# Performance work log

Measured on AMD Instinct MI355X. Metric: run time of the kernel, lower is better.

## Reference

```python
import jax, jax.numpy as jnp
import numpy as np

N = 4096      # nodes
DIM = 256     # in/out channels
H = 8         # heads
C = DIM       # per-head channels (PyG TransformerConv: out_channels per head)
EPS = 1e-5    # LayerNorm eps
P_EDGE = 0.01 # adjacency density -> avg in-degree ~41


def setup_inputs() -> dict:
    key = jax.random.key(0)
    ks = jax.random.split(key, 12)
    x = jax.random.normal(ks[0], (1, N, DIM), jnp.float32)
    # sparse random graph encoded densely (dense_to_sparse extracts nonzeros)
    adj_mat = (jax.random.uniform(ks[1], (1, N, N)) < P_EDGE).astype(jnp.float32)
    s = 1.0 / np.sqrt(DIM)
    Wq = jax.random.normal(ks[2], (DIM, H * C), jnp.float32) * s
    Wk = jax.random.normal(ks[3], (DIM, H * C), jnp.float32) * s
    Wv = jax.random.normal(ks[4], (DIM, H * C), jnp.float32) * s
    bq = jax.random.normal(ks[5], (H * C,), jnp.float32) * 0.01
    bk = jax.random.normal(ks[6], (H * C,), jnp.float32) * 0.01
    bv = jax.random.normal(ks[7], (H * C,), jnp.float32) * 0.01
    Wskip = jax.random.normal(ks[8], (DIM, DIM), jnp.float32) * s
    bskip = jax.random.normal(ks[9], (DIM,), jnp.float32) * 0.01
    gamma = jnp.ones((DIM,), jnp.float32)
    beta = jnp.zeros((DIM,), jnp.float32)
    return dict(x=x, adj_mat=adj_mat, Wq=Wq, bq=bq, Wk=Wk, bk=bk, Wv=Wv, bv=bv,
                Wskip=Wskip, bskip=bskip, gamma=gamma, beta=beta)


def reference(x, adj_mat, Wq, bq, Wk, bk, Wv, bv, Wskip, bskip, gamma, beta):
    xs = x[0]            # [N, DIM]
    adj = adj_mat[0]     # [N, N]; adj[j, i] != 0 => edge j -> i (source_to_target)
    q = (xs @ Wq + bq).reshape(N, H, C)
    k = (xs @ Wk + bk).reshape(N, H, C)
    v = (xs @ Wv + bv).reshape(N, H, C)
    # scaled dot-product attention restricted to graph edges
    scores = jnp.einsum('ihc,jhc->hij', q, k) / jnp.sqrt(jnp.float32(C))  # [H,N,N]
    mask = (adj.T != 0.0)[None]  # [1, i_target, j_source]
    neg = jnp.finfo(scores.dtype).min
    attn = jax.nn.softmax(jnp.where(mask, scores, neg), axis=-1)
    # nodes with no in-edges aggregate zero messages (scatter semantics)
    has_nbr = mask.any(axis=-1, keepdims=True)  # [1, N, 1]
    attn = jnp.where(has_nbr, attn, 0.0)
    agg = jnp.einsum('hij,jhc->ihc', attn, v)  # [N, H, C]
    out = agg.mean(axis=1)                      # concat=False -> head mean, [N, DIM]
    out = out + xs @ Wskip + bskip              # root_weight skip connection
    mu = out.mean(axis=-1, keepdims=True)
    var = ((out - mu) ** 2).mean(axis=-1, keepdims=True)
    out = (out - mu) * jax.lax.rsqrt(var + EPS) * gamma + beta  # LayerNorm
    out = out + xs                               # residual
    return out[None]  # [1, N, DIM]
```

## Files before the change

### kernel.cpp

```cpp
#include <hip/hip_runtime.h>
#include <hip/hip_bf16.h>

#define NN   4096
#define DIMM 256
#define HH   8
#define HC   2048
#define CAP  128

typedef short  bf16x8 __attribute__((ext_vector_type(8)));
typedef float  f32x4  __attribute__((ext_vector_type(4)));
typedef float  f32x2  __attribute__((ext_vector_type(2)));

__device__ __forceinline__ float bfbits(unsigned int u) {
  union { unsigned int u; float f; } un; un.u = u; return un.f;
}
__device__ __forceinline__ unsigned short f2bf(float f) {
  union { float f; unsigned int u; } un; un.f = f;
  unsigned int r = un.u + 0x7fffu + ((un.u >> 16) & 1u);
  return (unsigned short)(r >> 16);
}
__device__ __forceinline__ void gload16(const void* g, void* l) {
  __builtin_amdgcn_global_load_lds(
      (const __attribute__((address_space(1))) unsigned int*)g,
      (__attribute__((address_space(3))) unsigned int*)l, 16, 0, 0);
}

__global__ __launch_bounds__(256) void build_edges_kernel(
    const float4* __restrict__ adj4, int* __restrict__ deg, int* __restrict__ nbr) {
  const int stride = gridDim.x * blockDim.x;
  for (int e4 = blockIdx.x * blockDim.x + threadIdx.x; e4 < NN * NN / 4; e4 += stride) {
    const float4 a = adj4[e4];
    if (a.x != 0.f || a.y != 0.f || a.z != 0.f || a.w != 0.f) {
      const int e = e4 << 2;
      const int j = e >> 12;
      const int ib = e & (NN - 1);
      if (a.x != 0.f) { int s = atomicAdd(&deg[ib + 0], 1); if (s < CAP) nbr[(ib + 0) * CAP + s] = j; }
      if (a.y != 0.f) { int s = atomicAdd(&deg[ib + 1], 1); if (s < CAP) nbr[(ib + 1) * CAP + s] = j; }
      if (a.z != 0.f) { int s = atomicAdd(&deg[ib + 2], 1); if (s < CAP) nbr[(ib + 2) * CAP + s] = j; }
      if (a.w != 0.f) { int s = atomicAdd(&deg[ib + 3], 1); if (s < CAP) nbr[(ib + 3) * CAP + s] = j; }
    }
  }
}

__global__ __launch_bounds__(128) void sort_nbr_kernel(
    const int* __restrict__ deg, int* __restrict__ nbr) {
  const int i = blockIdx.x, t = threadIdx.x;
  __shared__ int sl[CAP];
  int d = deg[i];
  if (d > CAP) d = CAP;
  if (d <= 1) return;
  sl[t] = (t < d) ? nbr[i * CAP + t] : 0x7fffffff;
  __syncthreads();
  for (int ksz = 2; ksz <= CAP; ksz <<= 1) {
    for (int jsz = ksz >> 1; jsz > 0; jsz >>= 1) {
      const int ixj = t ^ jsz;
      if (ixj > t) {
        const int a = sl[t], b = sl[ixj];
        const bool up = ((t & ksz) == 0);
        if ((up && a > b) || (!up && a < b)) { sl[t] = b; sl[ixj] = a; }
      }
      __syncthreads();
    }
  }
  if (t < d) nbr[i * CAP + t] = sl[t];
}

__global__ __launch_bounds__(256) void cast_x_kernel(
    const float* __restrict__ x, unsigned short* __restrict__ xb) {
  const int gid = blockIdx.x * 256 + threadIdx.x;
  const int m = gid >> 5, c = gid & 31;
  const float4 a = *(const float4*)&x[(size_t)m * 256 + c * 8];
  const float4 b = *(const float4*)&x[(size_t)m * 256 + c * 8 + 4];
  union { unsigned short u[8]; uint4 v; } o;
  o.u[0] = f2bf(a.x); o.u[1] = f2bf(a.y); o.u[2] = f2bf(a.z); o.u[3] = f2bf(a.w);
  o.u[4] = f2bf(b.x); o.u[5] = f2bf(b.y); o.u[6] = f2bf(b.z); o.u[7] = f2bf(b.w);
  const int cs = (c & 24) | ((c & 7) ^ (m & 7));
  *(uint4*)&xb[(size_t)m * 256 + cs * 8] = o.v;
}

__global__ __launch_bounds__(256) void tcast_w_kernel(
    const float* __restrict__ W0, const float* __restrict__ W1,
    const float* __restrict__ W2, unsigned short* __restrict__ T0,
    unsigned short* __restrict__ T1, unsigned short* __restrict__ T2, int Nw) {
  const float* W = blockIdx.z == 0 ? W0 : blockIdx.z == 1 ? W1 : W2;
  unsigned short* T = blockIdx.z == 0 ? T0 : blockIdx.z == 1 ? T1 : T2;
  __shared__ float Tf[64][68];
  const int t = threadIdx.x;
  const int n0 = blockIdx.x * 64, k0 = blockIdx.y * 64;
  const int kk0 = t >> 4, nc = t & 15;
#pragma unroll
  for (int r = 0; r < 4; ++r) {
    const int kk = kk0 + r * 16;
    const float4 a = *(const float4*)&W[(size_t)(k0 + kk) * Nw + n0 + nc * 4];
    Tf[kk][nc * 4 + 0] = a.x; Tf[kk][nc * 4 + 1] = a.y;
    Tf[kk][nc * 4 + 2] = a.z; Tf[kk][nc * 4 + 3] = a.w;
  }
  __syncthreads();
  const int n = t >> 2, cp = t & 3;
#pragma unroll
  for (int qq = 0; qq < 2; ++qq) {
    const int cc = cp * 2 + qq;
    union { unsigned short u[8]; uint4 v; } o;
#pragma unroll
    for (int e = 0; e < 8; ++e) o.u[e] = f2bf(Tf[cc * 8 + e][n]);
    const int ng = n0 + n;
    const int co = cc ^ (ng & 7);
    *(uint4*)&T[(size_t)ng * 256 + blockIdx.y * 64 + co * 8] = o.v;
  }
}

template <int BF16OUT>
__global__ __launch_bounds__(256) void mfma_gemm_kernel(
    const unsigned short* __restrict__ Abf,
    const unsigned short* __restrict__ B0, const unsigned short* __restrict__ B1,
    const unsigned short* __restrict__ B2,
    const float* __restrict__ bias0, const float* __restrict__ bias1,
    const float* __restrict__ bias2,
    void* __restrict__ C0v, void* __restrict__ C1v, void* __restrict__ C2v,
    int Nc) {
  const unsigned short* Bm = blockIdx.z == 0 ? B0 : blockIdx.z == 1 ? B1 : B2;
  const float* bias = blockIdx.z == 0 ? bias0 : blockIdx.z == 1 ? bias1 : bias2;
  void* Cv = blockIdx.z == 0 ? C0v : blockIdx.z == 1 ? C1v : C2v;

  __shared__ unsigned short lds[2 * 128 * 64];
  unsigned short* As = lds;
  unsigned short* Bs = lds + 128 * 64;

  const int t = threadIdx.x, l = t & 63, w = t >> 6;
  const int m0 = blockIdx.y * 128, n0 = blockIdx.x * 128;
  const int wm = w >> 1, wn = w & 1;

  const f32x4 zero = {0.f, 0.f, 0.f, 0.f};
  f32x4 acc[4][4];
#pragma unroll
  for (int fm = 0; fm < 4; ++fm)
#pragma unroll
    for (int fn = 0; fn < 4; ++fn) acc[fm][fn] = zero;

  for (int kb = 0; kb < 4; ++kb) {
#pragma unroll
    for (int r = 0; r < 4; ++r) {
      const int rr = r * 8 + (l >> 3), ch = l & 7;
      gload16(Abf + (size_t)(m0 + w * 32 + rr) * 256 + kb * 64 + ch * 8,
              As + w * 2048 + r * 512);
      gload16(Bm + (size_t)(n0 + w * 32 + rr) * 256 + kb * 64 + ch * 8,
              Bs + w * 2048 + r * 512);
    }
    __syncthreads();

#pragma unroll
    for (int s = 0; s < 2; ++s) {
      const int chab = (4 * s + (l >> 4)) ^ (l & 7);
      bf16x8 af[4], bfr[4];
#pragma unroll
      for (int fm = 0; fm < 4; ++fm) {
        const int row = wm * 64 + fm * 16 + (l & 15);
        af[fm] = *(const bf16x8*)&As[row * 64 + chab * 8];
      }
#pragma unroll
      for (int fn = 0; fn < 4; ++fn) {
        const int row = wn * 64 + fn * 16 + (l & 15);
        bfr[fn] = *(const bf16x8*)&Bs[row * 64 + chab * 8];
      }
#pragma unroll
      for (int fm = 0; fm < 4; ++fm)
#pragma unroll
        for (int fn = 0; fn < 4; ++fn)
          acc[fm][fn] = __builtin_amdgcn_mfma_f32_16x16x32_bf16(
              af[fm], bfr[fn], acc[fm][fn], 0, 0, 0);
    }
    __syncthreads();
  }

  float bv[4];
#pragma unroll
  for (int fn = 0; fn < 4; ++fn) bv[fn] = bias[n0 + wn * 64 + fn * 16 + (l & 15)];

  if (BF16OUT) {
    unsigned short* Cc = (unsigned short*)Cv;
#pragma unroll
    for (int fm = 0; fm < 4; ++fm) {
      const int colc = wn * 64 + (l & 15);
#pragma unroll
      for (int fn = 0; fn < 4; ++fn) {
        const int col = colc + fn * 16;
#pragma unroll
        for (int r = 0; r < 4; ++r) {
          const int row = wm * 64 + fm * 16 + (l >> 4) * 4 + r;
          const int pos = ((col >> 3) ^ (row & 15)) * 8 + (col & 7);
          lds[row * 128 + pos] = f2bf(acc[fm][fn][r] + bv[fn]);
        }
      }
    }
    __syncthreads();
#pragma unroll
    for (int r2 = 0; r2 < 8; ++r2) {
      const int idx = r2 * 256 + t;
      const int row = idx >> 4, ch = idx & 15;
      *(uint4*)&Cc[(size_t)(m0 + row) * Nc + n0 + ch * 8] =
          *(const uint4*)&lds[row * 128 + (ch ^ (row & 15)) * 8];
    }
  } else {
    float* Cc = (float*)Cv;
#pragma unroll
    for (int fm = 0; fm < 4; ++fm)
#pragma unroll
      for (int fn = 0; fn < 4; ++fn)
#pragma unroll
        for (int r = 0; r < 4; ++r) {
          const int row = wm * 64 + fm * 16 + (l >> 4) * 4 + r;
          const int col = wn * 64 + fn * 16 + (l & 15);
          Cc[(size_t)(m0 + row) * Nc + n0 + col] = acc[fm][fn][r] + bv[fn];
        }
  }
}

__global__ __launch_bounds__(256) void cast8_kernel(
    const unsigned short* __restrict__ in, unsigned char* __restrict__ out8, int n8) {
  const int idx = blockIdx.x * 256 + threadIdx.x;
  if (idx >= n8) return;
  const uint4 w = *(const uint4*)&in[(size_t)idx * 8];
  const float f0 = bfbits(w.x << 16), f1 = bfbits(w.x & 0xffff0000u);
  const float f2 = bfbits(w.y << 16), f3 = bfbits(w.y & 0xffff0000u);
  const float f4 = bfbits(w.z << 16), f5 = bfbits(w.z & 0xffff0000u);
  const float f6 = bfbits(w.w << 16), f7 = bfbits(w.w & 0xffff0000u);
  unsigned int lo = __builtin_amdgcn_cvt_pk_fp8_f32(f0, f1, 0, false);
  lo = __builtin_amdgcn_cvt_pk_fp8_f32(f2, f3, lo, true);
  unsigned int hi = __builtin_amdgcn_cvt_pk_fp8_f32(f4, f5, 0, false);
  hi = __builtin_amdgcn_cvt_pk_fp8_f32(f6, f7, hi, true);
  uint2 o; o.x = lo; o.y = hi;
  *(uint2*)&out8[(size_t)idx * 8] = o;
}

__global__ __launch_bounds__(256) void attn_ln_kernel(
    const unsigned short* __restrict__ q, const unsigned char* __restrict__ k8,
    const unsigned char* __restrict__ v8, const float* __restrict__ skip,
    const float* __restrict__ x, const int* __restrict__ deg,
    const int* __restrict__ nbr, const float* __restrict__ gamma,
    const float* __restrict__ beta, float* __restrict__ out) {
  const int i = blockIdx.x;
  const int t = threadIdx.x;
  const int lane = t & 63, wave = t >> 6;
  const int h = lane >> 3, sub = lane & 7;

  __shared__ int slist[CAP];
  __shared__ float sc[CAP * HH];
  __shared__ float wacc[4][2][DIMM];
  __shared__ float mred[HH], lred[HH];
  __shared__ float w1[4], w2[4];

  int d = deg[i];
  if (d > CAP) d = CAP;

  if (t < CAP) slist[t] = (t < d) ? nbr[i * CAP + t] : 0;

  float qf[32];
  {
    const uint4* qp = (const uint4*)&q[(size_t)i * HC + (h << 8) + (sub << 5)];
#pragma unroll
    for (int b = 0; b < 4; ++b) {
      const uint4 w = qp[b];
      qf[b * 8 + 0] = bfbits(w.x << 16); qf[b * 8 + 1] = bfbits(w.x & 0xffff0000u);
      qf[b * 8 + 2] = bfbits(w.y << 16); qf[b * 8 + 3] = bfbits(w.y & 0xffff0000u);
      qf[b * 8 + 4] = bfbits(w.z << 16); qf[b * 8 + 5] = bfbits(w.z & 0xffff0000u);
      qf[b * 8 + 6] = bfbits(w.w << 16); qf[b * 8 + 7] = bfbits(w.w & 0xffff0000u);
    }
  }
  __syncthreads();

  {
    const size_t hoff = (size_t)(h << 8) + (sub << 5);
    int n = wave;
    uint4 c0, c1;
    if (n < d) {
      const uint4* kp = (const uint4*)&k8[(size_t)slist[n] * HC + hoff];
      c0 = kp[0]; c1 = kp[1];
    }
    while (n < d) {
      const int nn = n + 4;
      uint4 p0, p1;
      if (nn < d) {
        const uint4* kp = (const uint4*)&k8[(size_t)slist[nn] * HC + hoff];
        p0 = kp[0]; p1 = kp[1];
      }
      float s = 0.f;
      const unsigned int cw[8] = {c0.x, c0.y, c0.z, c0.w, c1.x, c1.y, c1.z, c1.w};
#pragma unroll
      for (int b = 0; b < 8; ++b) {
        const f32x2 lo = __builtin_amdgcn_cvt_pk_f32_fp8(cw[b], false);
        const f32x2 hi = __builtin_amdgcn_cvt_pk_f32_fp8(cw[b], true);
        s = fmaf(qf[b * 4 + 0], lo[0], s);
        s = fmaf(qf[b * 4 + 1], lo[1], s);
        s = fmaf(qf[b * 4 + 2], hi[0], s);
        s = fmaf(qf[b * 4 + 3], hi[1], s);
      }
      s += __shfl_xor(s, 1);
      s += __shfl_xor(s, 2);
      s += __shfl_xor(s, 4);
      if (sub == 0) sc[n * HH + h] = s * 0.0625f;
      c0 = p0; c1 = p1;
      n = nn;
    }
  }
  __syncthreads();

  if (t < 64) {
    const int h2 = t >> 3, s2 = t & 7;
    float m = -1e30f;
    for (int n2 = s2; n2 < d; n2 += 8) m = fmaxf(m, sc[n2 * HH + h2]);
    m = fmaxf(m, __shfl_xor(m, 1));
    m = fmaxf(m, __shfl_xor(m, 2));
    m = fmaxf(m, __shfl_xor(m, 4));
    float lsum = 0.f;
    for (int n2 = s2; n2 < d; n2 += 8) lsum += expf(sc[n2 * HH + h2] - m);
    lsum += __shfl_xor(lsum, 1);
    lsum += __shfl_xor(lsum, 2);
    lsum += __shfl_xor(lsum, 4);
    if (s2 == 0) { mred[h2] = m; lred[h2] = (lsum > 0.f) ? 1.f / lsum : 0.f; }
  }
  __syncthreads();

  for (int e = t; e < d * HH; e += 256) {
    const int hh = e & (HH - 1);
    sc[e] = expf(sc[e] - mred[hh]) * lred[hh];
  }
  __syncthreads();

  float a[8] = {0.f, 0.f, 0.f, 0.f, 0.f, 0.f, 0.f, 0.f};
  const int g = lane >> 5, c8 = lane & 31;
  {
    const size_t voff = (size_t)(g * 4) * 256 + (size_t)c8 * 8;
    int n = wave;
    uint2 d0, d1, d2, d3;
    if (n < d) {
      const unsigned char* vr = &v8[(size_t)slist[n] * HC + voff];
      d0 = *(const uint2*)(vr + 0 * 256); d1 = *(const uint2*)(vr + 1 * 256);
      d2 = *(const uint2*)(vr + 2 * 256); d3 = *(const uint2*)(vr + 3 * 256);
    }
    while (n < d) {
      const int nn = n + 4;
      uint2 e0, e1, e2, e3;
      if (nn < d) {
        const unsigned char* vr = &v8[(size_t)slist[nn] * HC + voff];
        e0 = *(const uint2*)(vr + 0 * 256); e1 = *(const uint2*)(vr + 1 * 256);
        e2 = *(const uint2*)(vr + 2 * 256); e3 = *(const uint2*)(vr + 3 * 256);
      }
      const float p0 = sc[n * HH + g * 4 + 0];
      const float p1 = sc[n * HH + g * 4 + 1];
      const float p2 = sc[n * HH + g * 4 + 2];
      const float p3 = sc[n * HH + g * 4 + 3];
#define AGG_HEAD(w, p)                                                \
      {                                                               \
        const f32x2 u01 = __builtin_amdgcn_cvt_pk_f32_fp8((w).x, false); \
        const f32x2 u23 = __builtin_amdgcn_cvt_pk_f32_fp8((w).x, true);  \
        const f32x2 u45 = __builtin_amdgcn_cvt_pk_f32_fp8((w).y, false); \
        const f32x2 u67 = __builtin_amdgcn_cvt_pk_f32_fp8((w).y, true);  \
        a[0] = fmaf(p, u01[0], a[0]); a[1] = fmaf(p, u01[1], a[1]);   \
        a[2] = fmaf(p, u23[0], a[2]); a[3] = fmaf(p, u23[1], a[3]);   \
        a[4] = fmaf(p, u45[0], a[4]); a[5] = fmaf(p, u45[1], a[5]);   \
        a[6] = fmaf(p, u67[0], a[6]); a[7] = fmaf(p, u67[1], a[7]);   \
      }
      AGG_HEAD(d0, p0) AGG_HEAD(d1, p1) AGG_HEAD(d2, p2) AGG_HEAD(d3, p3)
#undef AGG_HEAD
      d0 = e0; d1 = e1; d2 = e2; d3 = e3;
      n = nn;
    }
  }
#pragma unroll
  for (int e = 0; e < 8; ++e) wacc[wave][g][c8 * 8 + e] = a[e];
  __syncthreads();

  float accsum = 0.f;
#pragma unroll
  for (int w2 = 0; w2 < 4; ++w2) accsum += wacc[w2][0][t] + wacc[w2][1][t];
  const float oval = accsum * 0.125f + skip[(size_t)i * DIMM + t];

  float s1 = oval, s2 = oval * oval;
#pragma unroll
  for (int off = 32; off > 0; off >>= 1) {
    s1 += __shfl_xor(s1, off, 64);
    s2 += __shfl_xor(s2, off, 64);
  }
  if (lane == 0) { w1[wave] = s1; w2[wave] = s2; }
  __syncthreads();
  const float S1 = w1[0] + w1[1] + w1[2] + w1[3];
  const float S2 = w2[0] + w2[1] + w2[2] + w2[3];
  const float mu = S1 * (1.0f / 256.0f);
  const float var = S2 * (1.0f / 256.0f) - mu * mu;
  const float rst = rsqrtf(var + 1e-5f);

  out[(size_t)i * DIMM + t] =
      (oval - mu) * rst * gamma[t] + beta[t] + x[(size_t)i * DIMM + t];
}

extern "C" void kernel_launch(void* const* d_in, const int* in_sizes, int n_in,
                              void* d_out, int out_size, void* d_ws, size_t ws_size,
                              hipStream_t stream) {
  const float* x     = (const float*)d_in[0];
  const float* adj   = (const float*)d_in[1];
  const float* Wq    = (const float*)d_in[2];
  const float* bq    = (const float*)d_in[3];
  const float* Wk    = (const float*)d_in[4];
  const float* bk    = (const float*)d_in[5];
  const float* Wv    = (const float*)d_in[6];
  const float* bv    = (const float*)d_in[7];
  const float* Wskip = (const float*)d_in[8];
  const float* bskip = (const float*)d_in[9];
  const float* gamma = (const float*)d_in[10];
  const float* beta  = (const float*)d_in[11];
  float* out = (float*)d_out;

  char* ws = (char*)d_ws;
  unsigned short* xb  = (unsigned short*)ws;
  unsigned short* WqT = xb  + (size_t)NN * DIMM;
  unsigned short* WkT = WqT + (size_t)HC * DIMM;
  unsigned short* WvT = WkT + (size_t)HC * DIMM;
  unsigned short* WsT = WvT + (size_t)HC * DIMM;
  unsigned short* qb  = WsT + (size_t)DIMM * DIMM;
  unsigned short* kbf = qb  + (size_t)NN * HC;
  unsigned short* vbf = kbf + (size_t)NN * HC;
  float* skip = (float*)(vbf + (size_t)NN * HC);
  unsigned char* k8 = (unsigned char*)(skip + (size_t)NN * DIMM);
  unsigned char* v8 = k8 + (size_t)NN * HC;
  int* deg = (int*)(v8 + (size_t)NN * HC);
  int* nbr = deg + NN;

  hipMemsetAsync(deg, 0, NN * sizeof(int), stream);
  build_edges_kernel<<<2048, 256, 0, stream>>>((const float4*)adj, deg, nbr);
  sort_nbr_kernel<<<NN, 128, 0, stream>>>(deg, nbr);

  cast_x_kernel<<<NN * 32 / 256, 256, 0, stream>>>(x, xb);
  tcast_w_kernel<<<dim3(HC / 64, 4, 3), 256, 0, stream>>>(Wq, Wk, Wv, WqT, WkT, WvT, HC);
  tcast_w_kernel<<<dim3(DIMM / 64, 4, 1), 256, 0, stream>>>(Wskip, Wskip, Wskip,
                                                            WsT, WsT, WsT, DIMM);

  mfma_gemm_kernel<1><<<dim3(HC / 128, NN / 128, 3), 256, 0, stream>>>(
      xb, WqT, WkT, WvT, bq, bk, bv, qb, kbf, vbf, HC);
  mfma_gemm_kernel<0><<<dim3(DIMM / 128, NN / 128, 1), 256, 0, stream>>>(
      xb, WsT, WsT, WsT, bskip, bskip, bskip, skip, skip, skip, DIMM);

  cast8_kernel<<<(2 * NN * HC / 8 + 255) / 256, 256, 0, stream>>>(
      kbf, k8, 2 * NN * HC / 8);

  attn_ln_kernel<<<NN, 256, 0, stream>>>(qb, k8, v8, skip, x, deg, nbr,
                                         gamma, beta, out);
}
```

Baseline: 155.9 us.

## Fuse fp8 V cast into GEMM epilogue, use fp16 Q/K with dot2

The QKV GEMM epilogue now writes Q and K as fp16 and V directly as fp8, which removes the separate cast8 kernel and its extra pass over K and V in memory. The attention score loop reads fp16 K (twice the bytes of the old fp8 K) and uses packed fp16 dot2 instructions instead of fp8 unpacking plus scalar FMAs. This trades more K gather bandwidth for fewer conversions, one fewer launch, and higher K precision; fp16 may overflow for large activations.

```diff
diff --git a/kernel.cpp b/kernel.cpp
--- a/kernel.cpp
+++ b/kernel.cpp
@@ -7,9 +7,10 @@
 #define HC   2048
 #define CAP  128
 
-typedef short  bf16x8 __attribute__((ext_vector_type(8)));
-typedef float  f32x4  __attribute__((ext_vector_type(4)));
-typedef float  f32x2  __attribute__((ext_vector_type(2)));
+typedef short    bf16x8 __attribute__((ext_vector_type(8)));
+typedef float    f32x4  __attribute__((ext_vector_type(4)));
+typedef float    f32x2  __attribute__((ext_vector_type(2)));
+typedef _Float16 h2     __attribute__((ext_vector_type(2)));
 
 __device__ __forceinline__ float bfbits(unsigned int u) {
   union { unsigned int u; float f; } un; un.u = u; return un.f;
@@ -18,6 +19,19 @@
   union { float f; unsigned int u; } un; un.f = f;
   unsigned int r = un.u + 0x7fffu + ((un.u >> 16) & 1u);
   return (unsigned short)(r >> 16);
+}
+__device__ __forceinline__ unsigned short f2h(float f) {
+  union { _Float16 h; unsigned short u; } un; un.h = (_Float16)f; return un.u;
+}
+__device__ __forceinline__ float fdot2h(unsigned int a, unsigned int b, float c) {
+#if __has_builtin(__builtin_amdgcn_fdot2)
+  union { unsigned int u; h2 h; } ua, ub; ua.u = a; ub.u = b;
+  return __builtin_amdgcn_fdot2(ua.h, ub.h, c, false);
+#else
+  union { unsigned int u; _Float16 h[2]; } ua, ub; ua.u = a; ub.u = b;
+  c = fmaf((float)ua.h[0], (float)ub.h[0], c);
+  return fmaf((float)ua.h[1], (float)ub.h[1], c);
+#endif
 }
 __device__ __forceinline__ void gload16(const void* g, void* l) {
   __builtin_amdgcn_global_load_lds(
@@ -109,7 +123,7 @@
   }
 }
 
-template <int BF16OUT>
+template <int MODE>
 __global__ __launch_bounds__(256) void mfma_gemm_kernel(
     const unsigned short* __restrict__ Abf,
     const unsigned short* __restrict__ B0, const unsigned short* __restrict__ B1,
@@ -176,7 +190,7 @@
 #pragma unroll
   for (int fn = 0; fn < 4; ++fn) bv[fn] = bias[n0 + wn * 64 + fn * 16 + (l & 15)];
 
-  if (BF16OUT) {
+  if (MODE == 1 && blockIdx.z < 2) {
     unsigned short* Cc = (unsigned short*)Cv;
 #pragma unroll
     for (int fm = 0; fm < 4; ++fm) {
@@ -188,7 +202,7 @@
         for (int r = 0; r < 4; ++r) {
           const int row = wm * 64 + fm * 16 + (l >> 4) * 4 + r;
           const int pos = ((col >> 3) ^ (row & 15)) * 8 + (col & 7);
-          lds[row * 128 + pos] = f2bf(acc[fm][fn][r] + bv[fn]);
+          lds[row * 128 + pos] = f2h(acc[fm][fn][r] + bv[fn]);
         }
       }
     }
@@ -200,6 +214,31 @@
       *(uint4*)&Cc[(size_t)(m0 + row) * Nc + n0 + ch * 8] =
           *(const uint4*)&lds[row * 128 + (ch ^ (row & 15)) * 8];
     }
+  } else if (MODE == 1) {
+    unsigned char* lds8 = (unsigned char*)lds;
+    unsigned char* Cc8 = (unsigned char*)Cv;
+#pragma unroll
+    for (int fm = 0; fm < 4; ++fm) {
+      const int col = wn * 64 + (l & 15);
+#pragma unroll
+      for (int fn = 0; fn < 4; ++fn) {
+#pragma unroll
+        for (int r = 0; r < 4; ++r) {
+          const int row = wm * 64 + fm * 16 + (l >> 4) * 4 + r;
+          const float val = acc[fm][fn][r] + bv[fn];
+          const unsigned int pk = __builtin_amdgcn_cvt_pk_fp8_f32(val, val, 0, false);
+          lds8[row * 128 + col + fn * 16] = (unsigned char)(pk & 0xff);
+        }
+      }
+    }
+    __syncthreads();
+#pragma unroll
+    for (int r2 = 0; r2 < 4; ++r2) {
+      const int idx = r2 * 256 + t;
+      const int row = idx >> 3, colb = (idx & 7) * 16;
+      *(uint4*)&Cc8[(size_t)(m0 + row) * Nc + n0 + colb] =
+          *(const uint4*)&lds8[row * 128 + colb];
+    }
   } else {
     float* Cc = (float*)Cv;
 #pragma unroll
@@ -215,25 +254,8 @@
   }
 }
 
-__global__ __launch_bounds__(256) void cast8_kernel(
-    const unsigned short* __restrict__ in, unsigned char* __restrict__ out8, int n8) {
-  const int idx = blockIdx.x * 256 + threadIdx.x;
-  if (idx >= n8) return;
-  const uint4 w = *(const uint4*)&in[(size_t)idx * 8];
-  const float f0 = bfbits(w.x << 16), f1 = bfbits(w.x & 0xffff0000u);
-  const float f2 = bfbits(w.y << 16), f3 = bfbits(w.y & 0xffff0000u);
-  const float f4 = bfbits(w.z << 16), f5 = bfbits(w.z & 0xffff0000u);
-  const float f6 = bfbits(w.w << 16), f7 = bfbits(w.w & 0xffff0000u);
-  unsigned int lo = __builtin_amdgcn_cvt_pk_fp8_f32(f0, f1, 0, false);
-  lo = __builtin_amdgcn_cvt_pk_fp8_f32(f2, f3, lo, true);
-  unsigned int hi = __builtin_amdgcn_cvt_pk_fp8_f32(f4, f5, 0, false);
-  hi = __builtin_amdgcn_cvt_pk_fp8_f32(f6, f7, hi, true);
-  uint2 o; o.x = lo; o.y = hi;
-  *(uint2*)&out8[(size_t)idx * 8] = o;
-}
-
 __global__ __launch_bounds__(256) void attn_ln_kernel(
-    const unsigned short* __restrict__ q, const unsigned char* __restrict__ k8,
+    const unsigned short* __restrict__ q16, const unsigned short* __restrict__ k16,
     const unsigned char* __restrict__ v8, const float* __restrict__ skip,
     const float* __restrict__ x, const int* __restrict__ deg,
     const int* __restrict__ nbr, const float* __restrict__ gamma,
@@ -254,69 +276,60 @@
 
   if (t < CAP) slist[t] = (t < d) ? nbr[i * CAP + t] : 0;
 
-  float qf[32];
+  uint4 Q0, Q1, Q2, Q3;
   {
-    const uint4* qp = (const uint4*)&q[(size_t)i * HC + (h << 8) + (sub << 5)];
-#pragma unroll
-    for (int b = 0; b < 4; ++b) {
-      const uint4 w = qp[b];
-      qf[b * 8 + 0] = bfbits(w.x << 16); qf[b * 8 + 1] = bfbits(w.x & 0xffff0000u);
-      qf[b * 8 + 2] = bfbits(w.y << 16); qf[b * 8 + 3] = bfbits(w.y & 0xffff0000u);
-      qf[b * 8 + 4] = bfbits(w.z << 16); qf[b * 8 + 5] = bfbits(w.z & 0xffff0000u);
-      qf[b * 8 + 6] = bfbits(w.w << 16); qf[b * 8 + 7] = bfbits(w.w & 0xffff0000u);
-    }
+    const uint4* qp = (const uint4*)&q16[(size_t)i * HC + (h << 8) + (sub << 5)];
+    Q0 = qp[0]; Q1 = qp[1]; Q2 = qp[2]; Q3 = qp[3];
   }
   __syncthreads();
 
   {
     const size_t hoff = (size_t)(h << 8) + (sub << 5);
     int n = wave;
-    uint4 c0, c1;
+    uint4 c0, c1, c2, c3;
     if (n < d) {
-      const uint4* kp = (const uint4*)&k8[(size_t)slist[n] * HC + hoff];
-      c0 = kp[0]; c1 = kp[1];
+      const uint4* kp = (const uint4*)&k16[(size_t)slist[n] * HC + hoff];
+      c0 = kp[0]; c1 = kp[1]; c2 = kp[2]; c3 = kp[3];
     }
     while (n < d) {
       const int nn = n + 4;
-      uint4 p0, p1;
+      uint4 p0, p1, p2, p3;
       if (nn < d) {
-        const uint4* kp = (const uint4*)&k8[(size_t)slist[nn] * HC + hoff];
-        p0 = kp[0]; p1 = kp[1];
+        const uint4* kp = (const uint4*)&k16[(size_t)slist[nn] * HC + hoff];
+        p0 = kp[0]; p1 = kp[1]; p2 = kp[2]; p3 = kp[3];
       }
       float s = 0.f;
-      const unsigned int cw[8] = {c0.x, c0.y, c0.z, c0.w, c1.x, c1.y, c1.z, c1.w};
-#pragma unroll
-      for (int b = 0; b < 8; ++b) {
-        const f32x2 lo = __builtin_amdgcn_cvt_pk_f32_fp8(cw[b], false);
-        const f32x2 hi = __builtin_amdgcn_cvt_pk_f32_fp8(cw[b], true);
-        s = fmaf(qf[b * 4 + 0], lo[0], s);
-        s = fmaf(qf[b * 4 + 1], lo[1], s);
-        s = fmaf(qf[b * 4 + 2], hi[0], s);
-        s = fmaf(qf[b * 4 + 3], hi[1], s);
-      }
+      s = fdot2h(c0.x, Q0.x, s); s = fdot2h(c0.y, Q0.y, s);
+      s = fdot2h(c0.z, Q0.z, s); s = fdot2h(c0.w, Q0.w, s);
+      s = fdot2h(c1.x, Q1.x, s); s = fdot2h(c1.y, Q1.y, s);
+      s = fdot2h(c1.z, Q1.z, s); s = fdot2h(c1.w, Q1.w, s);
+      s = fdot2h(c2.x, Q2.x, s); s = fdot2h(c2.y, Q2.y, s);
+      s = fdot2h(c2.z, Q2.z, s); s = fdot2h(c2.w, Q2.w, s);
+      s = fdot2h(c3.x, Q3.x, s); s = fdot2h(c3.y, Q3.y, s);
+      s = fdot2h(c3.z, Q3.z, s); s = fdot2h(c3.w, Q3.w, s);
       s += __shfl_xor(s, 1);
       s += __shfl_xor(s, 2);
       s += __shfl_xor(s, 4);
       if (sub == 0) sc[n * HH + h] = s * 0.0625f;
-      c0 = p0; c1 = p1;
+      c0 = p0; c1 = p1; c2 = p2; c3 = p3;
       n = nn;
     }
   }
   __syncthreads();
 
   if (t < 64) {
-    const int h2 = t >> 3, s2 = t & 7;
+    const int h2i = t >> 3, s2 = t & 7;
     float m = -1e30f;
-    for (int n2 = s2; n2 < d; n2 += 8) m = fmaxf(m, sc[n2 * HH + h2]);
+    for (int n2 = s2; n2 < d; n2 += 8) m = fmaxf(m, sc[n2 * HH + h2i]);
     m = fmaxf(m, __shfl_xor(m, 1));
     m = fmaxf(m, __shfl_xor(m, 2));
     m = fmaxf(m, __shfl_xor(m, 4));
     float lsum = 0.f;
-    for (int n2 = s2; n2 < d; n2 += 8) lsum += expf(sc[n2 * HH + h2] - m);
+    for (int n2 = s2; n2 < d; n2 += 8) lsum += expf(sc[n2 * HH + h2i] - m);
     lsum += __shfl_xor(lsum, 1);
     lsum += __shfl_xor(lsum, 2);
     lsum += __shfl_xor(lsum, 4);
-    if (s2 == 0) { mred[h2] = m; lred[h2] = (lsum > 0.f) ? 1.f / lsum : 0.f; }
+    if (s2 == 0) { mred[h2i] = m; lred[h2i] = (lsum > 0.f) ? 1.f / lsum : 0.f; }
   }
   __syncthreads();
 
@@ -416,12 +429,10 @@
   unsigned short* WkT = WqT + (size_t)HC * DIMM;
   unsigned short* WvT = WkT + (size_t)HC * DIMM;
   unsigned short* WsT = WvT + (size_t)HC * DIMM;
-  unsigned short* qb  = WsT + (size_t)DIMM * DIMM;
-  unsigned short* kbf = qb  + (size_t)NN * HC;
-  unsigned short* vbf = kbf + (size_t)NN * HC;
-  float* skip = (float*)(vbf + (size_t)NN * HC);
-  unsigned char* k8 = (unsigned char*)(skip + (size_t)NN * DIMM);
-  unsigned char* v8 = k8 + (size_t)NN * HC;
+  unsigned short* q16 = WsT + (size_t)DIMM * DIMM;
+  unsigned short* k16 = q16 + (size_t)NN * HC;
+  float* skip = (float*)(k16 + (size_t)NN * HC);
+  unsigned char* v8 = (unsigned char*)(skip + (size_t)NN * DIMM);
   int* deg = (int*)(v8 + (size_t)NN * HC);
   int* nbr = deg + NN;
 
@@ -435,13 +446,10 @@
                                                             WsT, WsT, WsT, DIMM);
 
   mfma_gemm_kernel<1><<<dim3(HC / 128, NN / 128, 3), 256, 0, stream>>>(
-      xb, WqT, WkT, WvT, bq, bk, bv, qb, kbf, vbf, HC);
+      xb, WqT, WkT, WvT, bq, bk, bv, q16, k16, v8, HC);
   mfma_gemm_kernel<0><<<dim3(DIMM / 128, NN / 128, 1), 256, 0, stream>>>(
       xb, WsT, WsT, WsT, bskip, bskip, bskip, skip, skip, skip, DIMM);
 
-  cast8_kernel<<<(2 * NN * HC / 8 + 255) / 256, 256, 0, stream>>>(
-      kbf, k8, 2 * NN * HC / 8);
-
-  attn_ln_kernel<<<NN, 256, 0, stream>>>(qb, k8, v8, skip, x, deg, nbr,
+  attn_ln_kernel<<<NN, 256, 0, stream>>>(q16, k16, v8, skip, x, deg, nbr,
                                          gamma, beta, out);
 }
```

Measured after the change: 195.7 us. 25.5% more time.
